# Optimization experiments

Measured on AMD Instinct MI355X. Metric: run time of the kernel, lower is better.

Reference implementation:

```python
import jax, jax.numpy as jnp
import numpy as np

BS, C, H, W = 8, 64, 128, 128
KS = 3
SCALE = 2


def _pose_map(src_h, src_w, scale):
    # Vectorized version of positionKPN.pose_map (bilinear source coords).
    dst_h, dst_w = int(np.floor(src_h * scale)), int(np.floor(src_w * scale))
    scale_x, scale_y = float(src_w) / dst_w, float(src_h) / dst_h
    src_x = (np.arange(dst_w) + 0.5) * scale_x - 0.5
    src_y = (np.arange(dst_h) + 0.5) * scale_y - 0.5
    x0, y0 = np.floor(src_x), np.floor(src_y)
    inter_x = np.broadcast_to((x0 + 1).astype(np.int32)[None, :], (dst_h, dst_w))
    inter_y = np.broadcast_to((y0 + 1).astype(np.int32)[:, None], (dst_h, dst_w))
    fx = np.broadcast_to((src_x - x0).astype(np.float32)[None, :], (dst_h, dst_w))
    fy = np.broadcast_to((src_y - y0).astype(np.float32)[:, None], (dst_h, dst_w))
    pose = np.stack([fx, fy], axis=0).astype(np.float32)  # [2, dst_h, dst_w]
    return pose, np.ascontiguousarray(inter_y), np.ascontiguousarray(inter_x)


def setup_inputs() -> dict:
    key = jax.random.key(0)
    ks = jax.random.split(key, 8)
    pose, inter_y, inter_x = _pose_map(H, W, SCALE)
    s = 0.05
    return {
        "x": jax.random.normal(ks[0], (BS, C, H, W), dtype=jnp.float32),
        "scale": SCALE,
        "poseMap": jnp.asarray(pose),
        "interMapY": jnp.asarray(inter_y),
        "interMapX": jnp.asarray(inter_x),
        "W1": jax.random.normal(ks[1], (128, 2), dtype=jnp.float32) * s,
        "b1": jnp.zeros((128,), dtype=jnp.float32),
        "W2": jax.random.normal(ks[2], (256, 128), dtype=jnp.float32) * s,
        "b2": jnp.zeros((256,), dtype=jnp.float32),
        "W3": jax.random.normal(ks[3], (C * KS * KS, 256), dtype=jnp.float32) * s,
        "b3": jnp.zeros((C * KS * KS,), dtype=jnp.float32),
    }


def reference(x, scale, poseMap, interMapY, interMapX, W1, b1, W2, b2, W3, b3):
    bs, cs, h, w = x.shape
    ho, wo = interMapY.shape
    k2 = KS * KS
    # 1x1-conv MLP on position map -> per-pixel dynamic kernels.
    h1 = jax.nn.relu(jnp.einsum('oc,chw->ohw', W1, poseMap) + b1[:, None, None])
    h2 = jax.nn.relu(jnp.einsum('oc,chw->ohw', W2, h1) + b2[:, None, None])
    wgt = jnp.einsum('oc,chw->ohw', W3, h2) + b3[:, None, None]  # [cs*k2, ho, wo]
    wgt = wgt.reshape(cs, k2, ho, wo)
    # 3x3 patches gathered at source-grid centers interMap in [0, h] x [0, w]
    # (patch center y needs rows y-1..y+1 of x -> pad 1 before, 2 after).
    pad = KS // 2
    xp = jnp.pad(x, ((0, 0), (0, 0), (pad, pad + 1), (pad, pad + 1)))
    ky, kx = jnp.meshgrid(jnp.arange(KS), jnp.arange(KS), indexing='ij')
    Y = interMapY[None, :, :] + ky.reshape(k2, 1, 1)  # [k2, ho, wo]
    X = interMapX[None, :, :] + kx.reshape(k2, 1, 1)
    taps = xp[:, :, Y, X]  # [bs, cs, k2, ho, wo]
    out = jnp.einsum('bckyx,ckyx->bcyx', taps, wgt)  # per-pixel dynamic depthwise conv
    return out
```

## Files before the change

### kernel.cpp

```cpp
#include <hip/hip_runtime.h>

#define H_IN   128
#define W_IN   128
#define H_OUT  256
#define W_OUT  256
#define C_CH   64
#define B_SZ   8

typedef float vfloat4 __attribute__((ext_vector_type(4)));

__device__ __forceinline__ float rfl(float v) {
    return __uint_as_float(__builtin_amdgcn_readfirstlane(__float_as_uint(v)));
}

__global__ __launch_bounds__(576) void kpn_mlp(
    const float* __restrict__ pose,
    const float* __restrict__ W1,
    const float* __restrict__ b1,
    const float* __restrict__ W2,
    const float* __restrict__ b2,
    const float* __restrict__ W3,
    const float* __restrict__ b3,
    float* __restrict__ wgt4)
{
    __shared__ float h1[128];
    __shared__ float h2[256];

    const int p  = blockIdx.x;
    const int py = p >> 1, px = p & 1;
    const int t  = threadIdx.x;

    const float fx = pose[0 * H_OUT * W_OUT + py * W_OUT + px];
    const float fy = pose[1 * H_OUT * W_OUT + py * W_OUT + px];

    if (t < 128) {
        float a = W1[t * 2 + 0] * fx + W1[t * 2 + 1] * fy + b1[t];
        h1[t] = a > 0.f ? a : 0.f;
    }
    __syncthreads();

    if (t < 256) {
        float acc = b2[t];
        const float4* w = (const float4*)(W2 + t * 128);
        #pragma unroll 8
        for (int k = 0; k < 32; ++k) {
            float4 wv = w[k];
            acc += wv.x * h1[4 * k + 0] + wv.y * h1[4 * k + 1]
                 + wv.z * h1[4 * k + 2] + wv.w * h1[4 * k + 3];
        }
        h2[t] = acc > 0.f ? acc : 0.f;
    }
    __syncthreads();

    {
        float acc = b3[t];
        const float4* w = (const float4*)(W3 + t * 256);
        #pragma unroll 16
        for (int k = 0; k < 64; ++k) {
            float4 wv = w[k];
            acc += wv.x * h2[4 * k + 0] + wv.y * h2[4 * k + 1]
                 + wv.z * h2[4 * k + 2] + wv.w * h2[4 * k + 3];
        }
        const int c = t / 9, k = t - c * 9;
        wgt4[c * 48 + p * 12 + k] = acc;
    }
}

__global__ __launch_bounds__(256) void kpn_apply(
    const float* __restrict__ x,
    const float* __restrict__ wgt4,
    float* __restrict__ out)
{
    __shared__ float2 lds[H_IN][W_IN / 2];

    const int t  = threadIdx.x;
    const int l  = t & 63;
    const int wv = t >> 6;

    #pragma unroll 1
    for (int half = 0; half < 2; ++half) {
        const int bc = blockIdx.x + half * 256;
        const int c  = bc & 63;

        if (half) __syncthreads();
        {
            const float4* src = (const float4*)(x + (size_t)bc * (H_IN * W_IN));
            float4* dst = (float4*)&lds[0][0];
            #pragma unroll
            for (int k = 0; k < 16; ++k)
                dst[t + k * 256] = src[t + k * 256];
        }

        float wt[4][9];
        {
            const float* wp = wgt4 + c * 48;
            #pragma unroll
            for (int p = 0; p < 4; ++p) {
                float4 a = *(const float4*)(wp + p * 12);
                float4 b = *(const float4*)(wp + p * 12 + 4);
                float  g = wp[p * 12 + 8];
                wt[p][0] = rfl(a.x); wt[p][1] = rfl(a.y); wt[p][2] = rfl(a.z); wt[p][3] = rfl(a.w);
                wt[p][4] = rfl(b.x); wt[p][5] = rfl(b.y); wt[p][6] = rfl(b.z); wt[p][7] = rfl(b.w);
                wt[p][8] = rfl(g);
            }
        }
        __syncthreads();

        const int i0 = 32 * wv;

        float M[4], Ax[4], Bx[4], Dx[4], Ex[4];
        auto expand = [&](int r) {
            const bool ok = ((unsigned)r < (unsigned)H_IN);
            float ax = 0.f, bx = 0.f;
            if (ok) { float2 v = lds[r][l]; ax = v.x; bx = v.y; }
            float m = __shfl_up(bx, 1, 64);   if (l == 0)  m = 0.f;
            float d = __shfl_down(ax, 1, 64); if (l == 63) d = 0.f;
            float e = __shfl_down(bx, 1, 64); if (l == 63) e = 0.f;
            const int s = r & 3;
            M[s] = m; Ax[s] = ax; Bx[s] = bx; Dx[s] = d; Ex[s] = e;
        };

        expand(i0 - 1);
        expand(i0);
        expand(i0 + 1);

        float* op = out + ((size_t)bc * H_OUT + 2 * (size_t)i0) * W_OUT + 4 * l;

        #pragma unroll 4
        for (int q = i0; q < i0 + 32; ++q) {
            expand(q + 2);

            float ox0 = 0.f, ox1 = 0.f, ox2 = 0.f, ox3 = 0.f;
            float oy0 = 0.f, oy1 = 0.f, oy2 = 0.f, oy3 = 0.f;
            #pragma unroll
            for (int ky = 0; ky < 3; ++ky) {
                const int su = (q - 1 + ky) & 3;
                const int sl = (q + ky) & 3;
                const float w0a = wt[0][3*ky+0], w0b = wt[0][3*ky+1], w0c = wt[0][3*ky+2];
                const float w1a = wt[1][3*ky+0], w1b = wt[1][3*ky+1], w1c = wt[1][3*ky+2];
                const float w2a = wt[2][3*ky+0], w2b = wt[2][3*ky+1], w2c = wt[2][3*ky+2];
                const float w3a = wt[3][3*ky+0], w3b = wt[3][3*ky+1], w3c = wt[3][3*ky+2];
                ox0 += w0a * M[su]  + w0b * Ax[su] + w0c * Bx[su];
                ox1 += w1a * Ax[su] + w1b * Bx[su] + w1c * Dx[su];
                ox2 += w0a * Ax[su] + w0b * Bx[su] + w0c * Dx[su];
                ox3 += w1a * Bx[su] + w1b * Dx[su] + w1c * Ex[su];
                oy0 += w2a * M[sl]  + w2b * Ax[sl] + w2c * Bx[sl];
                oy1 += w3a * Ax[sl] + w3b * Bx[sl] + w3c * Dx[sl];
                oy2 += w2a * Ax[sl] + w2b * Bx[sl] + w2c * Dx[sl];
                oy3 += w3a * Bx[sl] + w3b * Dx[sl] + w3c * Ex[sl];
            }
            vfloat4 r0 = { ox0, ox1, ox2, ox3 };
            vfloat4 r1 = { oy0, oy1, oy2, oy3 };
            __builtin_nontemporal_store(r0, (vfloat4*)op);
            __builtin_nontemporal_store(r1, (vfloat4*)(op + W_OUT));
            op += 2 * W_OUT;
        }
    }
}

extern "C" void kernel_launch(void* const* d_in, const int* in_sizes, int n_in,
                              void* d_out, int out_size, void* d_ws, size_t ws_size,
                              hipStream_t stream) {
    const float* x      = (const float*)d_in[0];
    const float* pose   = (const float*)d_in[2];
    const float* W1     = (const float*)d_in[5];
    const float* b1     = (const float*)d_in[6];
    const float* W2     = (const float*)d_in[7];
    const float* b2     = (const float*)d_in[8];
    const float* W3     = (const float*)d_in[9];
    const float* b3     = (const float*)d_in[10];
    float*       out    = (float*)d_out;
    float*       wgt4   = (float*)d_ws;

    kpn_mlp<<<dim3(4), dim3(576), 0, stream>>>(pose, W1, b1, W2, b2, W3, b3, wgt4);
    kpn_apply<<<dim3(256), dim3(256), 0, stream>>>(x, wgt4, out);
}
```

Baseline: 59.47 us.

## Launch one 512-thread block per image-channel with interleaved row assignment

The apply kernel now uses 512 blocks of 512 threads, one (batch, channel) plane per block, instead of 256 blocks that each processed two planes in sequence. Each wave handles rows interleaved by 8 and reloads all four neighbouring LDS rows per output row, dropping the rolling row window. This is meant to raise parallelism and occupancy and remove the serialized second half. The cost is more LDS reads and shuffles per output row, since row reuse across iterations is lost.

```diff
diff --git a/kernel.cpp b/kernel.cpp
--- a/kernel.cpp
+++ b/kernel.cpp
@@ -66,7 +66,7 @@
     }
 }
 
-__global__ __launch_bounds__(256) void kpn_apply(
+__global__ __launch_bounds__(512, 4) void kpn_apply(
     const float* __restrict__ x,
     const float* __restrict__ wgt4,
     float* __restrict__ out)
@@ -76,85 +76,73 @@
     const int t  = threadIdx.x;
     const int l  = t & 63;
     const int wv = t >> 6;
+    const int bc = blockIdx.x;
+    const int c  = bc & 63;
 
-    #pragma unroll 1
-    for (int half = 0; half < 2; ++half) {
-        const int bc = blockIdx.x + half * 256;
-        const int c  = bc & 63;
+    {
+        const float4* src = (const float4*)(x + (size_t)bc * (H_IN * W_IN));
+        float4* dst = (float4*)&lds[0][0];
+        #pragma unroll
+        for (int k = 0; k < 8; ++k)
+            dst[t + k * 512] = src[t + k * 512];
+    }
 
-        if (half) __syncthreads();
-        {
-            const float4* src = (const float4*)(x + (size_t)bc * (H_IN * W_IN));
-            float4* dst = (float4*)&lds[0][0];
-            #pragma unroll
-            for (int k = 0; k < 16; ++k)
-                dst[t + k * 256] = src[t + k * 256];
+    float wt[4][9];
+    {
+        const float* wp = wgt4 + c * 48;
+        #pragma unroll
+        for (int p = 0; p < 4; ++p) {
+            float4 a = *(const float4*)(wp + p * 12);
+            float4 b = *(const float4*)(wp + p * 12 + 4);
+            float  g = wp[p * 12 + 8];
+            wt[p][0] = rfl(a.x); wt[p][1] = rfl(a.y); wt[p][2] = rfl(a.z); wt[p][3] = rfl(a.w);
+            wt[p][4] = rfl(b.x); wt[p][5] = rfl(b.y); wt[p][6] = rfl(b.z); wt[p][7] = rfl(b.w);
+            wt[p][8] = rfl(g);
         }
+    }
+    __syncthreads();
 
-        float wt[4][9];
-        {
-            const float* wp = wgt4 + c * 48;
-            #pragma unroll
-            for (int p = 0; p < 4; ++p) {
-                float4 a = *(const float4*)(wp + p * 12);
-                float4 b = *(const float4*)(wp + p * 12 + 4);
-                float  g = wp[p * 12 + 8];
-                wt[p][0] = rfl(a.x); wt[p][1] = rfl(a.y); wt[p][2] = rfl(a.z); wt[p][3] = rfl(a.w);
-                wt[p][4] = rfl(b.x); wt[p][5] = rfl(b.y); wt[p][6] = rfl(b.z); wt[p][7] = rfl(b.w);
-                wt[p][8] = rfl(g);
-            }
-        }
-        __syncthreads();
-
-        const int i0 = 32 * wv;
+    #pragma unroll 4
+    for (int k = 0; k < 16; ++k) {
+        const int i = 8 * k + wv;
 
         float M[4], Ax[4], Bx[4], Dx[4], Ex[4];
-        auto expand = [&](int r) {
-            const bool ok = ((unsigned)r < (unsigned)H_IN);
+        #pragma unroll
+        for (int r = 0; r < 4; ++r) {
+            const int rr = i - 1 + r;
+            const bool ok = ((unsigned)rr < (unsigned)H_IN);
             float ax = 0.f, bx = 0.f;
-            if (ok) { float2 v = lds[r][l]; ax = v.x; bx = v.y; }
+            if (ok) { float2 vv = lds[rr][l]; ax = vv.x; bx = vv.y; }
             float m = __shfl_up(bx, 1, 64);   if (l == 0)  m = 0.f;
             float d = __shfl_down(ax, 1, 64); if (l == 63) d = 0.f;
             float e = __shfl_down(bx, 1, 64); if (l == 63) e = 0.f;
-            const int s = r & 3;
-            M[s] = m; Ax[s] = ax; Bx[s] = bx; Dx[s] = d; Ex[s] = e;
-        };
+            M[r] = m; Ax[r] = ax; Bx[r] = bx; Dx[r] = d; Ex[r] = e;
+        }
 
-        expand(i0 - 1);
-        expand(i0);
-        expand(i0 + 1);
-
-        float* op = out + ((size_t)bc * H_OUT + 2 * (size_t)i0) * W_OUT + 4 * l;
-
-        #pragma unroll 4
-        for (int q = i0; q < i0 + 32; ++q) {
-            expand(q + 2);
-
-            float ox0 = 0.f, ox1 = 0.f, ox2 = 0.f, ox3 = 0.f;
-            float oy0 = 0.f, oy1 = 0.f, oy2 = 0.f, oy3 = 0.f;
-            #pragma unroll
-            for (int ky = 0; ky < 3; ++ky) {
-                const int su = (q - 1 + ky) & 3;
-                const int sl = (q + ky) & 3;
-                const float w0a = wt[0][3*ky+0], w0b = wt[0][3*ky+1], w0c = wt[0][3*ky+2];
-                const float w1a = wt[1][3*ky+0], w1b = wt[1][3*ky+1], w1c = wt[1][3*ky+2];
-                const float w2a = wt[2][3*ky+0], w2b = wt[2][3*ky+1], w2c = wt[2][3*ky+2];
-                const float w3a = wt[3][3*ky+0], w3b = wt[3][3*ky+1], w3c = wt[3][3*ky+2];
-                ox0 += w0a * M[su]  + w0b * Ax[su] + w0c * Bx[su];
-                ox1 += w1a * Ax[su] + w1b * Bx[su] + w1c * Dx[su];
-                ox2 += w0a * Ax[su] + w0b * Bx[su] + w0c * Dx[su];
-                ox3 += w1a * Bx[su] + w1b * Dx[su] + w1c * Ex[su];
-                oy0 += w2a * M[sl]  + w2b * Ax[sl] + w2c * Bx[sl];
-                oy1 += w3a * Ax[sl] + w3b * Bx[sl] + w3c * Dx[sl];
-                oy2 += w2a * Ax[sl] + w2b * Bx[sl] + w2c * Dx[sl];
-                oy3 += w3a * Bx[sl] + w3b * Dx[sl] + w3c * Ex[sl];
-            }
-            vfloat4 r0 = { ox0, ox1, ox2, ox3 };
-            vfloat4 r1 = { oy0, oy1, oy2, oy3 };
-            __builtin_nontemporal_store(r0, (vfloat4*)op);
-            __builtin_nontemporal_store(r1, (vfloat4*)(op + W_OUT));
-            op += 2 * W_OUT;
+        float ox0 = 0.f, ox1 = 0.f, ox2 = 0.f, ox3 = 0.f;
+        float oy0 = 0.f, oy1 = 0.f, oy2 = 0.f, oy3 = 0.f;
+        #pragma unroll
+        for (int ky = 0; ky < 3; ++ky) {
+            const int su = ky;
+            const int sl = ky + 1;
+            const float w0a = wt[0][3*ky+0], w0b = wt[0][3*ky+1], w0c = wt[0][3*ky+2];
+            const float w1a = wt[1][3*ky+0], w1b = wt[1][3*ky+1], w1c = wt[1][3*ky+2];
+            const float w2a = wt[2][3*ky+0], w2b = wt[2][3*ky+1], w2c = wt[2][3*ky+2];
+            const float w3a = wt[3][3*ky+0], w3b = wt[3][3*ky+1], w3c = wt[3][3*ky+2];
+            ox0 += w0a * M[su]  + w0b * Ax[su] + w0c * Bx[su];
+            ox1 += w1a * Ax[su] + w1b * Bx[su] + w1c * Dx[su];
+            ox2 += w0a * Ax[su] + w0b * Bx[su] + w0c * Dx[su];
+            ox3 += w1a * Bx[su] + w1b * Dx[su] + w1c * Ex[su];
+            oy0 += w2a * M[sl]  + w2b * Ax[sl] + w2c * Bx[sl];
+            oy1 += w3a * Ax[sl] + w3b * Bx[sl] + w3c * Dx[sl];
+            oy2 += w2a * Ax[sl] + w2b * Bx[sl] + w2c * Dx[sl];
+            oy3 += w3a * Bx[sl] + w3b * Dx[sl] + w3c * Ex[sl];
         }
+        float* op = out + ((size_t)bc * H_OUT + 2 * (size_t)i) * W_OUT + 4 * l;
+        vfloat4 r0 = { ox0, ox1, ox2, ox3 };
+        vfloat4 r1 = { oy0, oy1, oy2, oy3 };
+        __builtin_nontemporal_store(r0, (vfloat4*)op);
+        __builtin_nontemporal_store(r1, (vfloat4*)(op + W_OUT));
     }
 }
 
@@ -173,5 +161,5 @@
     float*       wgt4   = (float*)d_ws;
 
     kpn_mlp<<<dim3(4), dim3(576), 0, stream>>>(pose, W1, b1, W2, b2, W3, b3, wgt4);
-    kpn_apply<<<dim3(256), dim3(256), 0, stream>>>(x, wgt4, out);
+    kpn_apply<<<dim3(512), dim3(512), 0, stream>>>(x, wgt4, out);
 }
```

Measured after the change: 56.83 us. -4.4%, faster.
